# Performance work log

Measured on AMD Instinct MI355X. Metric: run time of the kernel, lower is better.

## Reference

```python
import jax, jax.numpy as jnp
import numpy as np

D_MODEL = 1024
NHEAD = 8
HEAD_DIM = D_MODEL // NHEAD
D_FF = 4096
EPS_ATTN = 1e-6
EPS_LN = 1e-5


def _layernorm(x, g, b):
    mu = jnp.mean(x, axis=-1, keepdims=True)
    var = jnp.var(x, axis=-1, keepdims=True)
    return (x - mu) * jax.lax.rsqrt(var + EPS_LN) * g + b


def _linear_attention(q, k, v):
    # q,k,v: [N, L, H, D]
    Q = jax.nn.elu(q) + 1.0
    K = jax.nn.elu(k) + 1.0
    v_length = v.shape[1]
    v = v / v_length
    KV = jnp.einsum('nshd,nshv->nhdv', K, v)           # [N,H,D,D]
    Z = 1.0 / (jnp.einsum('nlhd,nhd->nlh', Q, K.sum(axis=1)) + EPS_ATTN)
    out = jnp.einsum('nlhd,nhdv,nlh->nlhv', Q, KV, Z) * v_length
    return out


def setup_inputs() -> dict:
    key = jax.random.key(0)
    ks = jax.random.split(key, 12)
    s = 1.0 / np.sqrt(D_MODEL)
    sf = 1.0 / np.sqrt(D_FF)
    return {
        'x': jax.random.normal(ks[0], (2, 4096, D_MODEL), jnp.float32),
        'wq': jax.random.normal(ks[1], (D_MODEL, D_MODEL), jnp.float32) * s,
        'wk': jax.random.normal(ks[2], (D_MODEL, D_MODEL), jnp.float32) * s,
        'wv': jax.random.normal(ks[3], (D_MODEL, D_MODEL), jnp.float32) * s,
        'w1': jax.random.normal(ks[4], (D_FF, D_MODEL), jnp.float32) * s,
        'b1': jnp.zeros((D_FF,), jnp.float32),
        'w2': jax.random.normal(ks[5], (D_MODEL, D_FF), jnp.float32) * sf,
        'b2': jnp.zeros((D_MODEL,), jnp.float32),
        'g1': jnp.ones((D_MODEL,), jnp.float32),
        'be1': jnp.zeros((D_MODEL,), jnp.float32),
        'g2': jnp.ones((D_MODEL,), jnp.float32),
        'be2': jnp.zeros((D_MODEL,), jnp.float32),
    }


def reference(x, wq, wk, wv, w1, b1, w2, b2, g1, be1, g2, be2):
    N, L, C = x.shape
    # pre-norm self attention
    x2 = _layernorm(x, g1, be1)
    q = (x2 @ wq.T).reshape(N, L, NHEAD, HEAD_DIM)
    k = (x2 @ wk.T).reshape(N, L, NHEAD, HEAD_DIM)
    v = (x2 @ wv.T).reshape(N, L, NHEAD, HEAD_DIM)
    msg = _linear_attention(q, k, v).reshape(N, L, C)
    x = x + msg
    # MLP block
    x2 = _layernorm(x, g2, be2)
    h = jax.nn.gelu(x2 @ w1.T + b1, approximate=False)
    x = x + (h @ w2.T + b2)
    return x
```

## Files before the change

### kernel.cpp

```cpp
#include <hip/hip_runtime.h>
#include <hip/hip_bf16.h>
#include <math.h>

typedef __bf16 bf16x8 __attribute__((ext_vector_type(8)));
typedef float f32x4 __attribute__((ext_vector_type(4)));

#define DEVI __device__ __forceinline__

DEVI void gload_lds16(const __bf16* g, __bf16* l) {
    __builtin_amdgcn_global_load_lds(
        (const __attribute__((address_space(1))) void*)g,
        (__attribute__((address_space(3))) void*)l, 16, 0, 0);
}

__global__ void sniff_kernel(const unsigned short* __restrict__ x, int* flags) {
    const int tid = threadIdx.x;
    const unsigned short u = x[tid * 2];
    const int e = (u >> 7) & 0xFF;
    const int zero = (u == 0) ? 1 : 0;
    const int sane = ((e >= 0x71 && e <= 0x8E) || ((u & 0x7FFF) == 0)) ? 1 : 0;
    const unsigned long long mz = __ballot(zero != 0);
    const unsigned long long ms = __ballot(sane != 0);
    __shared__ int wz[4], wsn[4];
    if ((tid & 63) == 0) { wz[tid >> 6] = __popcll(mz); wsn[tid >> 6] = __popcll(ms); }
    __syncthreads();
    if (tid == 0) {
        const int nz = wz[0] + wz[1] + wz[2] + wz[3];
        const int ns = wsn[0] + wsn[1] + wsn[2] + wsn[3];
        flags[0] = (nz >= 192 || ns < 128) ? 1 : 0;
    }
}

__global__ __launch_bounds__(256) void convert_kernel(const void* __restrict__ src,
                                                      __bf16* __restrict__ dst, int n,
                                                      const int* __restrict__ flags) {
    const int i = (blockIdx.x * 256 + threadIdx.x) * 8;
    if (i >= n) return;
    if (flags[0]) {
        const float* s = (const float*)src;
        bf16x8 o;
#pragma unroll
        for (int j = 0; j < 8; j++) o[j] = (__bf16)s[i + j];
        *(bf16x8*)(dst + i) = o;
    } else {
        *(uint4*)(dst + i) = *(const uint4*)((const __bf16*)src + i);
    }
}

template <typename T>
__global__ __launch_bounds__(256) void ln_kernel(const T* __restrict__ x,
                                                 const __bf16* __restrict__ g,
                                                 const __bf16* __restrict__ b,
                                                 __bf16* __restrict__ out) {
    const size_t row = blockIdx.x;
    const T* xr = x + row * 1024;
    const int tid = threadIdx.x;
    float v[4];
#pragma unroll
    for (int i = 0; i < 4; i++) v[i] = (float)xr[tid * 4 + i];
    float s = v[0] + v[1] + v[2] + v[3];
    float s2 = v[0] * v[0] + v[1] * v[1] + v[2] * v[2] + v[3] * v[3];
#pragma unroll
    for (int m = 32; m >= 1; m >>= 1) {
        s += __shfl_xor(s, m, 64);
        s2 += __shfl_xor(s2, m, 64);
    }
    __shared__ float rs[4], rs2[4];
    const int wave = tid >> 6, lane = tid & 63;
    if (lane == 0) { rs[wave] = s; rs2[wave] = s2; }
    __syncthreads();
    s = rs[0] + rs[1] + rs[2] + rs[3];
    s2 = rs2[0] + rs2[1] + rs2[2] + rs2[3];
    const float mu = s * (1.0f / 1024.0f);
    const float var = s2 * (1.0f / 1024.0f) - mu * mu;
    const float inv = rsqrtf(var + 1e-5f);
#pragma unroll
    for (int i = 0; i < 4; i++) {
        const int c = tid * 4 + i;
        out[row * 1024 + c] = (__bf16)((v[i] - mu) * inv * (float)g[c] + (float)b[c]);
    }
}

enum { EP_NONE = 0, EP_ELU1 = 1, EP_BIAS_GELU = 2, EP_BIAS_RES = 3, EP_QKV = 4 };

#define READMM(RA, RB)                                                            \
    do {                                                                          \
        bf16x8 af_[BM / 32], bfv_[4];                                             \
        _Pragma("unroll") for (int i_ = 0; i_ < BM / 32; i_++)                    \
            af_[i_] = *(const bf16x8*)&RA[(wm * (BM / 2) + i_ * 16 + lm) * 32 + swz]; \
        _Pragma("unroll") for (int j_ = 0; j_ < 4; j_++)                          \
            bfv_[j_] = *(const bf16x8*)&RB[(wn * 64 + j_ * 16 + lm) * 32 + swz];  \
        _Pragma("unroll") for (int i_ = 0; i_ < BM / 32; i_++)                    \
            _Pragma("unroll") for (int j_ = 0; j_ < 4; j_++)                      \
                acc[i_][j_] = __builtin_amdgcn_mfma_f32_16x16x32_bf16(            \
                    af_[i_], bfv_[j_], acc[i_][j_], 0, 0, 0);                     \
    } while (0)

#define KBODY(RA, RB, SA, SB, TS)                                  \
    do {                                                           \
        if constexpr (BM == 128)                                   \
            asm volatile("s_waitcnt vmcnt(4)" ::: "memory");       \
        else                                                       \
            asm volatile("s_waitcnt vmcnt(3)" ::: "memory");       \
        __builtin_amdgcn_s_barrier();                              \
        __builtin_amdgcn_sched_barrier(0);                         \
        if ((TS) < nt) {                                           \
            const int k0_ = (TS) << 5;                             \
            gload_lds16(pa0 + k0_, &SA[tid * 8]);                  \
            if constexpr (BM == 128)                               \
                gload_lds16(pa1 + k0_, &SA[2048 + tid * 8]);       \
            gload_lds16(pb0 + k0_, &SB[tid * 8]);                  \
            gload_lds16(pb1 + k0_, &SB[2048 + tid * 8]);           \
        }                                                          \
        __builtin_amdgcn_s_setprio(1);                             \
        READMM(RA, RB);                                            \
        __builtin_amdgcn_s_setprio(0);                             \
    } while (0)

template <int EP, int BM, typename OutT>
__global__ __launch_bounds__(256, 3) void gemm_bt(
    const __bf16* __restrict__ A, const __bf16* __restrict__ B,
    const __bf16* __restrict__ bias, const float* __restrict__ resid,
    OutT* __restrict__ C, int M, int N, int K) {
    const int gx = gridDim.x, gy = gridDim.y;
    int bm = blockIdx.y, bn = blockIdx.x;
    {
        const int nwg = gx * gy;
        if ((gx & 7) == 0 && (nwg & 63) == 0) {
            const int bid = bm * gx + bn;
            const int perx = nwg >> 3;
            const int gid = (bid & 7) * perx + (bid >> 3);
            const int stg = gid >> 6, pos = gid & 63;
            const int stw = gx >> 3;
            bm = (stg / stw) * 8 + (pos >> 3);
            bn = (stg % stw) * 8 + (pos & 7);
        }
    }
    const int tid = threadIdx.x;
    const int wave = tid >> 6, lane = tid & 63;
    const int wm = wave & 1, wn = wave >> 1;
    const int lm = lane & 15, lq = lane >> 4;
    const int swz = (lq ^ ((lm >> 1) & 3)) * 8;

    __shared__ __align__(16) __bf16 As0[BM * 32];
    __shared__ __align__(16) __bf16 As1[BM * 32];
    __shared__ __align__(16) __bf16 As2[BM * 32];
    __shared__ __align__(16) __bf16 Bs0[128 * 32];
    __shared__ __align__(16) __bf16 Bs1[128 * 32];
    __shared__ __align__(16) __bf16 Bs2[128 * 32];

    f32x4 acc[BM / 32][4] = {};

    const int sr = tid >> 2;
    const int sc = (((tid & 3) ^ ((tid >> 3) & 3)) << 3);

    const __bf16* pa0 = A + (size_t)(bm * BM + sr) * K + sc;
    const __bf16* pa1 = pa0 + (size_t)(BM == 128 ? 64 : 0) * K;
    const __bf16* pb0 = B + (size_t)(bn * 128 + sr) * K + sc;
    const __bf16* pb1 = pb0 + (size_t)64 * K;

    const int nt = K >> 5;

    gload_lds16(pa0, &As0[tid * 8]);
    if constexpr (BM == 128) gload_lds16(pa1, &As0[2048 + tid * 8]);
    gload_lds16(pb0, &Bs0[tid * 8]);
    gload_lds16(pb1, &Bs0[2048 + tid * 8]);
    if (nt > 1) {
        gload_lds16(pa0 + 32, &As1[tid * 8]);
        if constexpr (BM == 128) gload_lds16(pa1 + 32, &As1[2048 + tid * 8]);
        gload_lds16(pb0 + 32, &Bs1[tid * 8]);
        gload_lds16(pb1 + 32, &Bs1[2048 + tid * 8]);
    }

    int t = 0;
    for (; t + 2 < nt; t += 3) {
        KBODY(As0, Bs0, As2, Bs2, t + 2);
        KBODY(As1, Bs1, As0, Bs0, t + 3);
        KBODY(As2, Bs2, As1, Bs1, t + 4);
    }
    if (t < nt) {
        asm volatile("s_waitcnt vmcnt(0)" ::: "memory");
        __builtin_amdgcn_s_barrier();
        __builtin_amdgcn_sched_barrier(0);
        READMM(As0, Bs0);
        t++;
        if (t < nt) { READMM(As1, Bs1); }
    }

    const int row0 = bm * BM + wm * (BM / 2);
    const int col0 = bn * 128 + wn * 64;
#pragma unroll
    for (int i = 0; i < BM / 32; i++) {
#pragma unroll
        for (int j = 0; j < 4; j++) {
            const int col = col0 + j * 16 + lm;
#pragma unroll
            for (int r = 0; r < 4; r++) {
                const int row = row0 + i * 16 + lq * 4 + r;
                float v = acc[i][j][r];
                if (EP == EP_QKV) {
                    float vv = (col < 2048) ? ((v > 0.0f) ? (v + 1.0f) : expf(v)) : v;
                    __bf16* dst = (col < 1024) ? (__bf16*)C
                                : (col < 2048) ? (__bf16*)const_cast<__bf16*>(bias)
                                               : (__bf16*)const_cast<float*>(resid);
                    dst[(size_t)row * 1024 + (col & 1023)] = (__bf16)vv;
                } else {
                    if (EP == EP_ELU1) {
                        v = (v > 0.0f) ? (v + 1.0f) : expf(v);
                    } else if (EP == EP_BIAS_GELU) {
                        v += (float)bias[col];
                        v = 0.5f * v * (1.0f + erff(v * 0.70710678118654752f));
                    } else if (EP == EP_BIAS_RES) {
                        v += (float)bias[col];
                        v += resid[(size_t)row * N + col];
                    }
                    C[(size_t)row * N + col] = (OutT)v;
                }
            }
        }
    }
}

__global__ __launch_bounds__(256) void kv_kernel(const __bf16* __restrict__ Kf,
                                                 const __bf16* __restrict__ Vf,
                                                 float* __restrict__ pkv,
                                                 float* __restrict__ pks) {
    const int nh = blockIdx.x, sc = blockIdx.y;
    const int n = nh >> 3, h = nh & 7;
    const int tid = threadIdx.x;
    const int tv = tid & 15, td = tid >> 4;
    __shared__ __align__(16) __bf16 Kt[32 * 128];
    __shared__ __align__(16) __bf16 Vt[32 * 128];
    float acc[8][8] = {};
    float ks[8] = {};
    const size_t rowbase = (size_t)n * 4096 + (size_t)sc * 256;
    for (int s0 = 0; s0 < 256; s0 += 32) {
#pragma unroll
        for (int rep = 0; rep < 2; rep++) {
            const int s = tid + rep * 256;
            const int r = s >> 4, cs = (s & 15) * 8;
            const size_t gidx = (rowbase + s0 + r) * 1024 + h * 128 + cs;
            *(bf16x8*)&Kt[r * 128 + cs] = *(const bf16x8*)&Kf[gidx];
            *(bf16x8*)&Vt[r * 128 + cs] = *(const bf16x8*)&Vf[gidx];
        }
        __syncthreads();
#pragma unroll 4
        for (int s = 0; s < 32; s++) {
            const bf16x8 k8 = *(const bf16x8*)&Kt[s * 128 + td * 8];
            const bf16x8 v8 = *(const bf16x8*)&Vt[s * 128 + tv * 8];
            float kk[8], vv[8];
#pragma unroll
            for (int i = 0; i < 8; i++) { kk[i] = (float)k8[i]; vv[i] = (float)v8[i]; }
#pragma unroll
            for (int i = 0; i < 8; i++) {
                ks[i] += kk[i];
#pragma unroll
                for (int j = 0; j < 8; j++) acc[i][j] += kk[i] * vv[j];
            }
        }
        __syncthreads();
    }
    float* dst = pkv + ((size_t)sc * 16 + nh) * 16384;
#pragma unroll
    for (int i = 0; i < 8; i++)
#pragma unroll
        for (int j = 0; j < 8; j++)
            dst[(td * 8 + i) * 128 + tv * 8 + j] = acc[i][j];
    if (tv == 0) {
        float* ds2 = pks + ((size_t)sc * 16 + nh) * 128;
#pragma unroll
        for (int i = 0; i < 8; i++) ds2[td * 8 + i] = ks[i];
    }
}

__global__ __launch_bounds__(256) void kv_reduce(const float* __restrict__ pkv,
                                                 const float* __restrict__ pks,
                                                 __bf16* __restrict__ kvb,
                                                 float* __restrict__ ksf) {
    const int idx = blockIdx.x * 256 + threadIdx.x;
    float s = 0.0f;
#pragma unroll
    for (int c = 0; c < 16; c++) s += pkv[(size_t)c * 262144 + idx];
    kvb[idx] = (__bf16)s;
    if (idx < 2048) {
        float t = 0.0f;
#pragma unroll
        for (int c = 0; c < 16; c++) t += pks[c * 2048 + idx];
        ksf[idx] = t;
    }
}

__global__ __launch_bounds__(256, 2) void attn_out_kernel(
    const __bf16* __restrict__ x, const __bf16* __restrict__ Qf,
    const __bf16* __restrict__ kvb, const float* __restrict__ ksf,
    float* __restrict__ xmid) {
    const int nh = blockIdx.x, lc = blockIdx.y;
    const int n = nh >> 3, h = nh & 7;
    const int tid = threadIdx.x;
    __shared__ __align__(16) __bf16 KVs[128 * 128];
    __shared__ __align__(16) __bf16 Qs[64 * 128];
    __shared__ float Ks[128];
    const __bf16* kv = kvb + (size_t)nh * 16384;
    for (int i = tid * 8; i < 16384; i += 2048)
        *(bf16x8*)&KVs[i] = *(const bf16x8*)&kv[i];
    const size_t gr0 = (size_t)n * 4096 + (size_t)lc * 64;
#pragma unroll
    for (int rep = 0; rep < 4; rep++) {
        const int s = tid + rep * 256;
        const int r = s >> 4, cs = (s & 15) * 8;
        *(bf16x8*)&Qs[r * 128 + cs] = *(const bf16x8*)&Qf[(gr0 + r) * 1024 + h * 128 + cs];
    }
    if (tid < 128) Ks[tid] = ksf[(size_t)nh * 128 + tid];
    __syncthreads();
    const int tv = (tid & 15) * 8;
    const int tr0 = (tid >> 4) * 4;
    float acc[4][8] = {};
    float zs[4] = {};
    for (int d = 0; d < 128; d++) {
        const bf16x8 kv8 = *(const bf16x8*)&KVs[d * 128 + tv];
        const float ksd = Ks[d];
        float kf[8];
#pragma unroll
        for (int j = 0; j < 8; j++) kf[j] = (float)kv8[j];
#pragma unroll
        for (int rr = 0; rr < 4; rr++) {
            const float q = (float)Qs[(tr0 + rr) * 128 + d];
            zs[rr] += q * ksd;
#pragma unroll
            for (int j = 0; j < 8; j++) acc[rr][j] += q * kf[j];
        }
    }
#pragma unroll
    for (int rr = 0; rr < 4; rr++) {
        const size_t gi = (gr0 + tr0 + rr) * 1024 + h * 128 + tv;
        const float z = 1.0f / (zs[rr] + 1e-6f);
        const bf16x8 xr = *(const bf16x8*)&x[gi];
#pragma unroll
        for (int j = 0; j < 8; j++) xmid[gi + j] = (float)xr[j] + acc[rr][j] * z;
    }
}

extern "C" void kernel_launch(void* const* d_in, const int* in_sizes, int n_in,
                              void* d_out, int out_size, void* d_ws, size_t ws_size,
                              hipStream_t stream) {
    float* out = (float*)d_out;
    char* ws = (char*)d_ws;

    const int nx = 8388608, nw = 1048576, nw1 = 4194304, nb1 = 4096, ng = 1024;
    size_t off = 0;
    __bf16* cx   = (__bf16*)(ws + off); off += (size_t)nx * 2;
    __bf16* cwq  = (__bf16*)(ws + off); off += (size_t)nw * 2;
    __bf16* cwk  = (__bf16*)(ws + off); off += (size_t)nw * 2;
    __bf16* cwv  = (__bf16*)(ws + off); off += (size_t)nw * 2;
    __bf16* cw1  = (__bf16*)(ws + off); off += (size_t)nw1 * 2;
    __bf16* cb1  = (__bf16*)(ws + off); off += (size_t)nb1 * 2;
    __bf16* cw2  = (__bf16*)(ws + off); off += (size_t)nw1 * 2;
    __bf16* cb2  = (__bf16*)(ws + off); off += (size_t)ng * 2;
    __bf16* cg1  = (__bf16*)(ws + off); off += (size_t)ng * 2;
    __bf16* cbe1 = (__bf16*)(ws + off); off += (size_t)ng * 2;
    __bf16* cg2  = (__bf16*)(ws + off); off += (size_t)ng * 2;
    __bf16* cbe2 = (__bf16*)(ws + off); off += (size_t)ng * 2;
    int* flags = (int*)(ws + off); off += 64;

    char* PB = ws + off;
    __bf16* x2   = (__bf16*)(PB);
    __bf16* Qf   = (__bf16*)(PB + 16777216);
    float*  pkv  = (float*)(PB + 33554432);
    __bf16* hbuf = (__bf16*)(PB + 16777216);
    __bf16* Kf   = (__bf16*)(PB + 50331648);
    __bf16* Vf   = (__bf16*)(PB + 67108864);
    float*  xmid = (float*)(PB + 50331648);
    float*  pks  = (float*)(PB + 83886080);
    float*  ksf  = (float*)(PB + 84017152);
    __bf16* kvb  = (__bf16*)(PB + 84287488);

    sniff_kernel<<<1, 256, 0, stream>>>((const unsigned short*)d_in[0], flags);
    convert_kernel<<<nx / 2048, 256, 0, stream>>>(d_in[0], cx, nx, flags);
    convert_kernel<<<nw / 2048, 256, 0, stream>>>(d_in[1], cwq, nw, flags);
    convert_kernel<<<nw / 2048, 256, 0, stream>>>(d_in[2], cwk, nw, flags);
    convert_kernel<<<nw / 2048, 256, 0, stream>>>(d_in[3], cwv, nw, flags);
    convert_kernel<<<nw1 / 2048, 256, 0, stream>>>(d_in[4], cw1, nw1, flags);
    convert_kernel<<<2, 256, 0, stream>>>(d_in[5], cb1, nb1, flags);
    convert_kernel<<<nw1 / 2048, 256, 0, stream>>>(d_in[6], cw2, nw1, flags);
    convert_kernel<<<1, 256, 0, stream>>>(d_in[7], cb2, ng, flags);
    convert_kernel<<<1, 256, 0, stream>>>(d_in[8], cg1, ng, flags);
    convert_kernel<<<1, 256, 0, stream>>>(d_in[9], cbe1, ng, flags);
    convert_kernel<<<1, 256, 0, stream>>>(d_in[10], cg2, ng, flags);
    convert_kernel<<<1, 256, 0, stream>>>(d_in[11], cbe2, ng, flags);

    ln_kernel<__bf16><<<8192, 256, 0, stream>>>(cx, cg1, cbe1, x2);
    gemm_bt<EP_QKV, 128, __bf16><<<dim3(3072 / 128, 8192 / 128), 256, 0, stream>>>(
        x2, cwq, (const __bf16*)Kf, (const float*)Vf, Qf, 8192, 3072, 1024);
    kv_kernel<<<dim3(16, 16), 256, 0, stream>>>(Kf, Vf, pkv, pks);
    kv_reduce<<<1024, 256, 0, stream>>>(pkv, pks, kvb, ksf);
    attn_out_kernel<<<dim3(16, 64), 256, 0, stream>>>(cx, Qf, kvb, ksf, xmid);
    ln_kernel<float><<<8192, 256, 0, stream>>>(xmid, cg2, cbe2, x2);
    for (int c = 0; c < 2; c++) {
        const size_t ro = (size_t)c * 4096;
        gemm_bt<EP_BIAS_GELU, 128, __bf16><<<dim3(4096 / 128, 4096 / 128), 256, 0, stream>>>(
            x2 + ro * 1024, cw1, cb1, nullptr, hbuf, 4096, 4096, 1024);
        gemm_bt<EP_BIAS_RES, 64, float><<<dim3(1024 / 128, 4096 / 64), 256, 0, stream>>>(
            hbuf, cw2, cb2, xmid + ro * 1024, out + ro * 1024, 4096, 1024, 4096);
    }
}
```

Before: 441.7 us.

## Fuse input conversions, read fp32 x directly, and atomically reduce KV partials

When inputs are fp32, the separate sniff and per-tensor convert launches are replaced by one fused conversion kernel covering all weights. The x tensor is no longer converted: layernorm and the residual add read fp32 x directly. The kv_reduce pass is removed by having kv_kernel atomically accumulate into zeroed fp32 buffers, with the bf16 conversion moved into attn_out's LDS load. This cuts launch count and one round trip over x, in exchange for two memsets, atomic contention, and a non-deterministic summation order.

```diff
diff --git a/kernel.cpp b/kernel.cpp
--- a/kernel.cpp
+++ b/kernel.cpp
@@ -45,6 +45,27 @@
     } else {
         *(uint4*)(dst + i) = *(const uint4*)((const __bf16*)src + i);
     }
+}
+
+struct CvtJobs {
+    const float* s[11];
+    __bf16* d[11];
+    int n[11];
+    int b0[11];
+};
+__global__ __launch_bounds__(256) void convert_fused(CvtJobs J) {
+    const int bid = blockIdx.x;
+    int j = 0;
+#pragma unroll
+    for (int k = 1; k < 11; k++)
+        if (bid >= J.b0[k]) j = k;
+    const int i = (bid - J.b0[j]) * 2048 + threadIdx.x * 8;
+    if (i >= J.n[j]) return;
+    const float* s = J.s[j] + i;
+    bf16x8 o;
+#pragma unroll
+    for (int t = 0; t < 8; t++) o[t] = (__bf16)s[t];
+    *(bf16x8*)(J.d[j] + i) = o;
 }
 
 template <typename T>
@@ -223,8 +244,8 @@
 
 __global__ __launch_bounds__(256) void kv_kernel(const __bf16* __restrict__ Kf,
                                                  const __bf16* __restrict__ Vf,
-                                                 float* __restrict__ pkv,
-                                                 float* __restrict__ pks) {
+                                                 float* __restrict__ kvf,
+                                                 float* __restrict__ ksf) {
     const int nh = blockIdx.x, sc = blockIdx.y;
     const int n = nh >> 3, h = nh & 7;
     const int tid = threadIdx.x;
@@ -260,39 +281,23 @@
         }
         __syncthreads();
     }
-    float* dst = pkv + ((size_t)sc * 16 + nh) * 16384;
+    float* dst = kvf + (size_t)nh * 16384;
 #pragma unroll
     for (int i = 0; i < 8; i++)
 #pragma unroll
         for (int j = 0; j < 8; j++)
-            dst[(td * 8 + i) * 128 + tv * 8 + j] = acc[i][j];
+            atomicAdd(&dst[(td * 8 + i) * 128 + tv * 8 + j], acc[i][j]);
     if (tv == 0) {
-        float* ds2 = pks + ((size_t)sc * 16 + nh) * 128;
-#pragma unroll
-        for (int i = 0; i < 8; i++) ds2[td * 8 + i] = ks[i];
-    }
-}
-
-__global__ __launch_bounds__(256) void kv_reduce(const float* __restrict__ pkv,
-                                                 const float* __restrict__ pks,
-                                                 __bf16* __restrict__ kvb,
-                                                 float* __restrict__ ksf) {
-    const int idx = blockIdx.x * 256 + threadIdx.x;
-    float s = 0.0f;
-#pragma unroll
-    for (int c = 0; c < 16; c++) s += pkv[(size_t)c * 262144 + idx];
-    kvb[idx] = (__bf16)s;
-    if (idx < 2048) {
-        float t = 0.0f;
-#pragma unroll
-        for (int c = 0; c < 16; c++) t += pks[c * 2048 + idx];
-        ksf[idx] = t;
-    }
-}
-
+        float* ds2 = ksf + (size_t)nh * 128;
+#pragma unroll
+        for (int i = 0; i < 8; i++) atomicAdd(&ds2[td * 8 + i], ks[i]);
+    }
+}
+
+template <typename XT>
 __global__ __launch_bounds__(256, 2) void attn_out_kernel(
-    const __bf16* __restrict__ x, const __bf16* __restrict__ Qf,
-    const __bf16* __restrict__ kvb, const float* __restrict__ ksf,
+    const XT* __restrict__ x, const __bf16* __restrict__ Qf,
+    const float* __restrict__ kvf, const float* __restrict__ ksf,
     float* __restrict__ xmid) {
     const int nh = blockIdx.x, lc = blockIdx.y;
     const int n = nh >> 3, h = nh & 7;
@@ -300,9 +305,15 @@
     __shared__ __align__(16) __bf16 KVs[128 * 128];
     __shared__ __align__(16) __bf16 Qs[64 * 128];
     __shared__ float Ks[128];
-    const __bf16* kv = kvb + (size_t)nh * 16384;
-    for (int i = tid * 8; i < 16384; i += 2048)
-        *(bf16x8*)&KVs[i] = *(const bf16x8*)&kv[i];
+    const float* kv = kvf + (size_t)nh * 16384;
+    for (int i = tid * 8; i < 16384; i += 2048) {
+        const float4 u0 = *(const float4*)&kv[i];
+        const float4 u1 = *(const float4*)&kv[i + 4];
+        bf16x8 o;
+        o[0] = (__bf16)u0.x; o[1] = (__bf16)u0.y; o[2] = (__bf16)u0.z; o[3] = (__bf16)u0.w;
+        o[4] = (__bf16)u1.x; o[5] = (__bf16)u1.y; o[6] = (__bf16)u1.z; o[7] = (__bf16)u1.w;
+        *(bf16x8*)&KVs[i] = o;
+    }
     const size_t gr0 = (size_t)n * 4096 + (size_t)lc * 64;
 #pragma unroll
     for (int rep = 0; rep < 4; rep++) {
@@ -334,7 +345,7 @@
     for (int rr = 0; rr < 4; rr++) {
         const size_t gi = (gr0 + tr0 + rr) * 1024 + h * 128 + tv;
         const float z = 1.0f / (zs[rr] + 1e-6f);
-        const bf16x8 xr = *(const bf16x8*)&x[gi];
+        const XT* xr = x + gi;
 #pragma unroll
         for (int j = 0; j < 8; j++) xmid[gi + j] = (float)xr[j] + acc[rr][j] * z;
     }
@@ -365,35 +376,65 @@
     char* PB = ws + off;
     __bf16* x2   = (__bf16*)(PB);
     __bf16* Qf   = (__bf16*)(PB + 16777216);
-    float*  pkv  = (float*)(PB + 33554432);
+    float*  kvf  = (float*)(PB + 33554432);
     __bf16* hbuf = (__bf16*)(PB + 16777216);
     __bf16* Kf   = (__bf16*)(PB + 50331648);
     __bf16* Vf   = (__bf16*)(PB + 67108864);
     float*  xmid = (float*)(PB + 50331648);
-    float*  pks  = (float*)(PB + 83886080);
     float*  ksf  = (float*)(PB + 84017152);
-    __bf16* kvb  = (__bf16*)(PB + 84287488);
-
-    sniff_kernel<<<1, 256, 0, stream>>>((const unsigned short*)d_in[0], flags);
-    convert_kernel<<<nx / 2048, 256, 0, stream>>>(d_in[0], cx, nx, flags);
-    convert_kernel<<<nw / 2048, 256, 0, stream>>>(d_in[1], cwq, nw, flags);
-    convert_kernel<<<nw / 2048, 256, 0, stream>>>(d_in[2], cwk, nw, flags);
-    convert_kernel<<<nw / 2048, 256, 0, stream>>>(d_in[3], cwv, nw, flags);
-    convert_kernel<<<nw1 / 2048, 256, 0, stream>>>(d_in[4], cw1, nw1, flags);
-    convert_kernel<<<2, 256, 0, stream>>>(d_in[5], cb1, nb1, flags);
-    convert_kernel<<<nw1 / 2048, 256, 0, stream>>>(d_in[6], cw2, nw1, flags);
-    convert_kernel<<<1, 256, 0, stream>>>(d_in[7], cb2, ng, flags);
-    convert_kernel<<<1, 256, 0, stream>>>(d_in[8], cg1, ng, flags);
-    convert_kernel<<<1, 256, 0, stream>>>(d_in[9], cbe1, ng, flags);
-    convert_kernel<<<1, 256, 0, stream>>>(d_in[10], cg2, ng, flags);
-    convert_kernel<<<1, 256, 0, stream>>>(d_in[11], cbe2, ng, flags);
-
-    ln_kernel<__bf16><<<8192, 256, 0, stream>>>(cx, cg1, cbe1, x2);
+
+    const bool is_f32 = (in_sizes[0] == nx * 4);
+    if (is_f32) {
+        CvtJobs J;
+        const float* srcs[11] = {(const float*)d_in[1], (const float*)d_in[2],
+                                 (const float*)d_in[3], (const float*)d_in[4],
+                                 (const float*)d_in[5], (const float*)d_in[6],
+                                 (const float*)d_in[7], (const float*)d_in[8],
+                                 (const float*)d_in[9], (const float*)d_in[10],
+                                 (const float*)d_in[11]};
+        __bf16* dsts[11] = {cwq, cwk, cwv, cw1, cb1, cw2, cb2, cg1, cbe1, cg2, cbe2};
+        int ns[11] = {nw, nw, nw, nw1, nb1, nw1, ng, ng, ng, ng, ng};
+        int b = 0;
+        for (int k = 0; k < 11; k++) {
+            J.s[k] = srcs[k]; J.d[k] = dsts[k]; J.n[k] = ns[k]; J.b0[k] = b;
+            b += (ns[k] + 2047) / 2048;
+        }
+        convert_fused<<<b, 256, 0, stream>>>(J);
+    } else {
+        sniff_kernel<<<1, 256, 0, stream>>>((const unsigned short*)d_in[0], flags);
+        convert_kernel<<<nx / 2048, 256, 0, stream>>>(d_in[0], cx, nx, flags);
+        convert_kernel<<<nw / 2048, 256, 0, stream>>>(d_in[1], cwq, nw, flags);
+        convert_kernel<<<nw / 2048, 256, 0, stream>>>(d_in[2], cwk, nw, flags);
+        convert_kernel<<<nw / 2048, 256, 0, stream>>>(d_in[3], cwv, nw, flags);
+        convert_kernel<<<nw1 / 2048, 256, 0, stream>>>(d_in[4], cw1, nw1, flags);
+        convert_kernel<<<2, 256, 0, stream>>>(d_in[5], cb1, nb1, flags);
+        convert_kernel<<<nw1 / 2048, 256, 0, stream>>>(d_in[6], cw2, nw1, flags);
+        convert_kernel<<<1, 256, 0, stream>>>(d_in[7], cb2, ng, flags);
+        convert_kernel<<<1, 256, 0, stream>>>(d_in[8], cg1, ng, flags);
+        convert_kernel<<<1, 256, 0, stream>>>(d_in[9], cbe1, ng, flags);
+        convert_kernel<<<1, 256, 0, stream>>>(d_in[10], cg2, ng, flags);
+        convert_kernel<<<1, 256, 0, stream>>>(d_in[11], cbe2, ng, flags);
+    }
+
+    if (is_f32)
+        ln_kernel<float><<<8192, 256, 0, stream>>>((const float*)d_in[0], cg1, cbe1, x2);
+    else
+        ln_kernel<__bf16><<<8192, 256, 0, stream>>>(cx, cg1, cbe1, x2);
+
     gemm_bt<EP_QKV, 128, __bf16><<<dim3(3072 / 128, 8192 / 128), 256, 0, stream>>>(
         x2, cwq, (const __bf16*)Kf, (const float*)Vf, Qf, 8192, 3072, 1024);
-    kv_kernel<<<dim3(16, 16), 256, 0, stream>>>(Kf, Vf, pkv, pks);
-    kv_reduce<<<1024, 256, 0, stream>>>(pkv, pks, kvb, ksf);
-    attn_out_kernel<<<dim3(16, 64), 256, 0, stream>>>(cx, Qf, kvb, ksf, xmid);
+
+    hipMemsetAsync(kvf, 0, (size_t)262144 * 4, stream);
+    hipMemsetAsync(ksf, 0, (size_t)2048 * 4, stream);
+    kv_kernel<<<dim3(16, 16), 256, 0, stream>>>(Kf, Vf, kvf, ksf);
+
+    if (is_f32)
+        attn_out_kernel<float><<<dim3(16, 64), 256, 0, stream>>>(
+            (const float*)d_in[0], Qf, kvf, ksf, xmid);
+    else
+        attn_out_kernel<__bf16><<<dim3(16, 64), 256, 0, stream>>>(
+            cx, Qf, kvf, ksf, xmid);
+
     ln_kernel<float><<<8192, 256, 0, stream>>>(xmid, cg2, cbe2, x2);
     for (int c = 0; c < 2; c++) {
         const size_t ro = (size_t)c * 4096;
```

After: 551.1 us. 1.25x slower.
